# Kernel optimization log

Measured on AMD Instinct MI355X. Metric: run time of the kernel, lower is better.

Reference implementation:

```python
import jax, jax.numpy as jnp
import numpy as np

D, NH, B, N, P = 512, 4, 4096, 30, 30  # embed_dim, num_heads, batch, seq, num_positional_embeddings


def _ln(x, g, b, eps=1e-5):
    mu = jnp.mean(x, axis=-1, keepdims=True)
    var = jnp.mean((x - mu) ** 2, axis=-1, keepdims=True)
    return g * (x - mu) / jnp.sqrt(var + eps) + b


def setup_inputs() -> dict:
    key = jax.random.key(0)
    ks = jax.random.split(key, 8)
    s = 0.02
    x = jax.random.normal(ks[0], (B, N, D), jnp.float32)
    attention_mask = jnp.zeros((B, N), dtype=bool)
    order = jax.random.randint(ks[1], (B, N), 0, P)
    num_docs = jnp.full((B,), float(N), jnp.float32)
    docs_weights = jax.random.uniform(ks[2], (B, N), jnp.float32)
    clusters_centroids = jax.random.normal(ks[3], (B, D), jnp.float32)
    pos_emb = (jax.random.normal(ks[4], (P + 1, D), jnp.float32) * s).at[P].set(0.0)
    fc1_w1 = jax.random.normal(ks[5], (2 * D + 1, D), jnp.float32) * s
    fc1_b1 = jnp.zeros((D,), jnp.float32)
    fc1_w2 = jax.random.normal(ks[6], (D, NH), jnp.float32) * s
    fc1_b2 = jnp.zeros((NH,), jnp.float32)
    fc2_w = jax.random.normal(ks[7], (NH * D, D), jnp.float32) * s
    fc2_b = jnp.zeros((D,), jnp.float32)
    return dict(
        x=x, attention_mask=attention_mask, order=order, num_docs=num_docs,
        docs_weights=docs_weights, clusters_centroids=clusters_centroids,
        pos_emb=pos_emb, fc1_w1=fc1_w1, fc1_b1=fc1_b1, fc1_w2=fc1_w2, fc1_b2=fc1_b2,
        fc2_w=fc2_w, fc2_b=fc2_b,
        ln1_g=jnp.ones((D,), jnp.float32), ln1_b=jnp.zeros((D,), jnp.float32),
        ln2_g=jnp.ones((NH * D,), jnp.float32), ln2_b=jnp.zeros((NH * D,), jnp.float32),
        ln3_g=jnp.ones((D,), jnp.float32), ln3_b=jnp.zeros((D,), jnp.float32),
        ln4_g=jnp.ones((D,), jnp.float32), ln4_b=jnp.zeros((D,), jnp.float32),
    )


def reference(x, attention_mask, order, num_docs, docs_weights, clusters_centroids,
              pos_emb, fc1_w1, fc1_b1, fc1_w2, fc1_b2, fc2_w, fc2_b,
              ln1_g, ln1_b, ln2_g, ln2_b, ln3_g, ln3_b, ln4_g, ln4_b):
    eps = 1e-8
    # norm_1: F.normalize(x, dim=2, eps=1e-8)
    xn = x / jnp.maximum(jnp.linalg.norm(x, axis=2, keepdims=True), eps)
    # input layernorm
    x1 = _ln(xn, ln1_g, ln1_b)
    xp = x1 + pos_emb[order]  # [B,N,D]
    # weighted mean pool of x_positions
    mp = jnp.sum(xp * docs_weights[:, :, None], axis=1, keepdims=True) / num_docs[:, None, None]  # [B,1,D]
    # cosine similarity between mean_pool and each token (torch eps=1e-8)
    num = jnp.sum(mp * xp, axis=2)  # [B,N]
    den = jnp.maximum(jnp.linalg.norm(mp, axis=2) * jnp.linalg.norm(xp, axis=2), eps)
    cos = (num / den)[:, :, None]  # [B,N,1]
    fc1_in = jnp.concatenate([xp, jnp.broadcast_to(mp, xp.shape), cos], axis=2)  # [B,N,2D+1]
    Z = jnp.tanh(fc1_in @ fc1_w1 + fc1_b1) @ fc1_w2 + fc1_b2  # [B,N,H]
    Z = jnp.where(attention_mask[:, :, None], -jnp.inf, Z)
    A = jax.nn.softmax(Z, axis=1)  # [B,N,H]
    b, n, h = A.shape
    d = x1.shape[2]
    # Faithful to the original reshape([B*H, N, 1]) on a [B,N,H]-contiguous tensor
    A_h = A.reshape(b, h, n)
    Hh = jnp.einsum('bhn,bnd->bhd', A_h, x1).reshape(b, h * d)  # [B, H*D]
    # residual: weighted mean pool of x (post ln1), tiled per head
    mpx = jnp.sum(x1 * docs_weights[:, :, None], axis=1) / num_docs[:, None]  # [B,D]
    Hh = _ln(Hh + jnp.tile(mpx, (1, h)), ln2_g, ln2_b)
    pred = _ln(Hh @ fc2_w + fc2_b, ln3_g, ln3_b)  # afterFC layernorm
    pred = _ln(pred + jnp.mean(Hh.reshape(b, h, d), axis=1), ln4_g, ln4_b)
    return pred
```

## Files before the change

### kernel.cpp

```cpp
#include <hip/hip_runtime.h>
#include <hip/hip_bf16.h>

#define B_ 4096
#define N_ 30
#define D_ 512
#define H_ 4
#define M_ (B_*N_)
#define PE_ROWS 31

typedef unsigned short u16;
typedef __attribute__((ext_vector_type(8))) short bf16x8;
typedef __attribute__((ext_vector_type(4))) float f32x4;

__device__ __forceinline__ float bf2f(u16 s) { return __uint_as_float(((unsigned)s) << 16); }
__device__ __forceinline__ u16 f2bf(float f) {
  __hip_bfloat16 h = __float2bfloat16(f);
  return *reinterpret_cast<u16*>(&h);
}

__device__ __forceinline__ float ftanh(float x) {
  float e = __expf(2.f * x);
  return 1.f - 2.f * __builtin_amdgcn_rcpf(e + 1.f);
}

__device__ __forceinline__ void gll16(const void* g, void* l) {
  __builtin_amdgcn_global_load_lds(
      (const __attribute__((address_space(1))) unsigned int*)g,
      (__attribute__((address_space(3))) unsigned int*)l, 16, 0, 0);
}

__device__ __forceinline__ float wsum(float v) {
  #pragma unroll
  for (int m = 32; m >= 1; m >>= 1) v += __shfl_xor(v, m);
  return v;
}
__device__ __forceinline__ float wmax(float v) {
  #pragma unroll
  for (int m = 32; m >= 1; m >>= 1) v = fmaxf(v, __shfl_xor(v, m));
  return v;
}

__global__ __launch_bounds__(512) void k1_prep(
    const float* __restrict__ x, const int* __restrict__ order,
    const float* __restrict__ ndocs, const float* __restrict__ dw,
    const float* __restrict__ pe, const float* __restrict__ g1,
    const float* __restrict__ bln1,
    u16* __restrict__ x1bf, u16* __restrict__ mpbf, float* __restrict__ mpx,
    float* __restrict__ cosb) {
  __shared__ float lds_mp[8*512];
  __shared__ float lds_mpx[8*512];
  __shared__ float xps[32];
  int b = blockIdx.x;
  int tid = threadIdx.x;
  int wid = tid >> 6, lane = tid & 63;
  int d0 = lane * 8;
  float g[8], bl[8];
  *(float4*)&g[0]  = *(const float4*)&g1[d0];
  *(float4*)&g[4]  = *(const float4*)&g1[d0+4];
  *(float4*)&bl[0] = *(const float4*)&bln1[d0];
  *(float4*)&bl[4] = *(const float4*)&bln1[d0+4];
  float xp_reg[4][8];
  float accmp[8] = {0,0,0,0,0,0,0,0}, accmpx[8] = {0,0,0,0,0,0,0,0};
  #pragma unroll
  for (int t = 0; t < 4; ++t) {
    int n = wid + 8*t;
    if (n < N_) {
      int tok = b*N_ + n;
      float v[8];
      *(float4*)&v[0] = *(const float4*)&x[(size_t)tok*D_ + d0];
      *(float4*)&v[4] = *(const float4*)&x[(size_t)tok*D_ + d0 + 4];
      float ss = 0.f, sm = 0.f;
      #pragma unroll
      for (int i = 0; i < 8; ++i) { ss += v[i]*v[i]; sm += v[i]; }
      ss = wsum(ss); sm = wsum(sm);
      float inv = 1.f / fmaxf(sqrtf(ss), 1e-8f);
      float mu = sm * inv * (1.f/D_);
      float m2 = ss*inv*inv*(1.f/D_);
      float rs = 1.f / sqrtf(m2 - mu*mu + 1e-5f);
      int o = order[tok];
      float p8[8];
      *(float4*)&p8[0] = *(const float4*)&pe[(size_t)o*D_ + d0];
      *(float4*)&p8[4] = *(const float4*)&pe[(size_t)o*D_ + d0 + 4];
      float wv = dw[tok];
      float sq = 0.f;
      bf16x8 xb;
      #pragma unroll
      for (int i = 0; i < 8; ++i) {
        float x1v = g[i]*((v[i]*inv - mu)*rs) + bl[i];
        xb[i] = (short)f2bf(x1v);
        float xpv = x1v + p8[i];
        xp_reg[t][i] = xpv;
        accmp[i]  += wv*xpv;
        accmpx[i] += wv*x1v;
        sq += xpv*xpv;
      }
      *(bf16x8*)&x1bf[(size_t)tok*D_ + d0] = xb;
      sq = wsum(sq);
      if (lane == 0) xps[n] = sq;
    }
  }
  #pragma unroll
  for (int i = 0; i < 8; i += 4) {
    *(float4*)&lds_mp[wid*512 + d0 + i]  = *(float4*)&accmp[i];
    *(float4*)&lds_mpx[wid*512 + d0 + i] = *(float4*)&accmpx[i];
  }
  __syncthreads();
  float invnd = 1.f / ndocs[b];
  float mpv[8] = {0,0,0,0,0,0,0,0}, mpxv[8] = {0,0,0,0,0,0,0,0};
  #pragma unroll
  for (int w = 0; w < 8; ++w) {
    #pragma unroll
    for (int i = 0; i < 8; i += 4) {
      float4 a = *(float4*)&lds_mp[w*512 + d0 + i];
      mpv[i+0] += a.x; mpv[i+1] += a.y; mpv[i+2] += a.z; mpv[i+3] += a.w;
      float4 c = *(float4*)&lds_mpx[w*512 + d0 + i];
      mpxv[i+0] += c.x; mpxv[i+1] += c.y; mpxv[i+2] += c.z; mpxv[i+3] += c.w;
    }
  }
  #pragma unroll
  for (int i = 0; i < 8; ++i) { mpv[i] *= invnd; mpxv[i] *= invnd; }
  if (wid == 0) {
    bf16x8 mb;
    #pragma unroll
    for (int i = 0; i < 8; ++i) mb[i] = (short)f2bf(mpv[i]);
    *(bf16x8*)&mpbf[(size_t)b*D_ + d0] = mb;
  }
  if (wid == 1) {
    #pragma unroll
    for (int i = 0; i < 8; i += 4)
      *(float4*)&mpx[(size_t)b*D_ + d0 + i] = *(float4*)&mpxv[i];
  }
  float mn = 0.f;
  #pragma unroll
  for (int i = 0; i < 8; ++i) mn += mpv[i]*mpv[i];
  float mpn = sqrtf(wsum(mn));
  #pragma unroll
  for (int t = 0; t < 4; ++t) {
    int n = wid + 8*t;
    if (n < N_) {
      float dot = 0.f;
      #pragma unroll
      for (int i = 0; i < 8; ++i) dot += mpv[i]*xp_reg[t][i];
      dot = wsum(dot);
      if (lane == 0)
        cosb[b*N_ + n] = dot / fmaxf(mpn * sqrtf(xps[n]), 1e-8f);
    }
  }
}

__global__ __launch_bounds__(512) void k_pew(
    const float* __restrict__ pe, const float* __restrict__ w1,
    float* __restrict__ peW) {
  int p = blockIdx.x, j = threadIdx.x;
  float acc = 0.f;
  for (int dd = 0; dd < D_; ++dd) acc += pe[p*D_ + dd] * w1[(size_t)dd*D_ + j];
  peW[p*D_ + j] = acc;
}

__global__ __launch_bounds__(256) void k_tcvt(
    const float* __restrict__ in, u16* __restrict__ out, int Kdim, int Jdim) {
  __shared__ float tile[64][65];
  int k0 = blockIdx.x * 64, j0 = blockIdx.y * 64;
  int t = threadIdx.x;
  int tr = t >> 4, tc4 = (t & 15) * 4;
  #pragma unroll
  for (int i = 0; i < 4; ++i) {
    int k = k0 + tr + i*16;
    float4 v = *(const float4*)&in[(size_t)k*Jdim + j0 + tc4];
    tile[tr + i*16][tc4+0] = v.x;
    tile[tr + i*16][tc4+1] = v.y;
    tile[tr + i*16][tc4+2] = v.z;
    tile[tr + i*16][tc4+3] = v.w;
  }
  __syncthreads();
  #pragma unroll
  for (int i = 0; i < 4; ++i) {
    int j = tr + i*16;
    uint2 u;
    u.x = (unsigned)f2bf(tile[tc4+0][j]) | ((unsigned)f2bf(tile[tc4+1][j]) << 16);
    u.y = (unsigned)f2bf(tile[tc4+2][j]) | ((unsigned)f2bf(tile[tc4+3][j]) << 16);
    *(uint2*)&out[(size_t)(j0+j)*Kdim + k0 + tc4] = u;
  }
}

__global__ __launch_bounds__(256, 3) void k2_mpw(
    const u16* __restrict__ mpbf, const u16* __restrict__ w1mT,
    const float* __restrict__ b1, float* __restrict__ mpW) {
  __shared__ __align__(16) u16 As[128*64];
  __shared__ __align__(16) u16 Bs[128*64];
  int tid = threadIdx.x;
  int lane = tid & 63, wid = tid >> 6;
  int wg = (blockIdx.x & 7)*16 + (blockIdx.x >> 3);
  int colb = wg & 3, rowb = wg >> 2;
  int row0 = rowb*128, col0 = colb*128;
  int wm = wid >> 1, wn = wid & 1;
  int lr = lane & 15, lk = lane >> 4;
  int srow = lane >> 3;
  int skel = ((lane & 7) ^ srow) << 3;
  f32x4 acc[4][4];
  #pragma unroll
  for (int nf = 0; nf < 4; ++nf) {
    float bv = b1[col0 + wn*64 + nf*16 + lr];
    #pragma unroll
    for (int mf = 0; mf < 4; ++mf)
      acc[mf][nf] = (f32x4){bv, bv, bv, bv};
  }
  for (int k0 = 0; k0 < D_; k0 += 64) {
    __syncthreads();
    #pragma unroll
    for (int i = 0; i < 4; ++i) {
      int rb = wid*32 + i*8;
      gll16(&mpbf[(size_t)(row0 + rb + srow)*D_ + k0 + skel], &As[rb*64]);
      gll16(&w1mT[(size_t)(col0 + rb + srow)*D_ + k0 + skel], &Bs[rb*64]);
    }
    __syncthreads();
    #pragma unroll
    for (int kk = 0; kk < 2; ++kk) {
      int kb = (kk*64 + lk*16) ^ ((lr & 7) << 4);
      bf16x8 a[4];
      #pragma unroll
      for (int mf = 0; mf < 4; ++mf)
        a[mf] = *(const bf16x8*)((const char*)As + (wm*64 + mf*16 + lr)*128 + kb);
      #pragma unroll
      for (int nf = 0; nf < 4; ++nf) {
        bf16x8 bfr = *(const bf16x8*)((const char*)Bs + (wn*64 + nf*16 + lr)*128 + kb);
        #pragma unroll
        for (int mf = 0; mf < 4; ++mf)
          acc[mf][nf] = __builtin_amdgcn_mfma_f32_16x16x32_bf16(a[mf], bfr, acc[mf][nf], 0, 0, 0);
      }
    }
  }
  #pragma unroll
  for (int mf = 0; mf < 4; ++mf)
    #pragma unroll
    for (int nf = 0; nf < 4; ++nf)
      #pragma unroll
      for (int r = 0; r < 4; ++r) {
        int m = row0 + wm*64 + mf*16 + lk*4 + r;
        int j = col0 + wn*64 + nf*16 + lr;
        mpW[(size_t)m*D_ + j] = acc[mf][nf][r];
      }
}

__global__ __launch_bounds__(256, 3) void k4_fc1(
    const u16* __restrict__ x1bf, const u16* __restrict__ w1T,
    const float* __restrict__ w1, const float* __restrict__ w2,
    const int* __restrict__ order, const float* __restrict__ cosb,
    const float* __restrict__ mpW, const float* __restrict__ peW,
    float* __restrict__ Zp) {
  __shared__ __align__(16) u16 As[128*64];
  __shared__ __align__(16) u16 Bs[128*64];
  __shared__ float zred[2*128*4];
  int tid = threadIdx.x;
  int lane = tid & 63, wid = tid >> 6;
  int wg = (blockIdx.x & 7)*480 + (blockIdx.x >> 3);
  int colb = wg & 3, rowb = wg >> 2;
  int col0 = colb * 128;
  int row0 = rowb * 128;
  int wm = wid >> 1, wn = wid & 1;
  int lr = lane & 15, lk = lane >> 4;
  int srow = lane >> 3;
  int skel = ((lane & 7) ^ srow) << 3;
  float wl[4];
  #pragma unroll
  for (int nf = 0; nf < 4; ++nf)
    wl[nf] = w1[(size_t)1024*D_ + col0 + wn*64 + nf*16 + lr];
  f32x4 acc[4][4];
  #pragma unroll
  for (int mf = 0; mf < 4; ++mf) {
    #pragma unroll
    for (int r = 0; r < 4; ++r) {
      int m = row0 + wm*64 + mf*16 + lk*4 + r;
      int bidx = m / N_;
      int o = order[m];
      float cs = cosb[m];
      #pragma unroll
      for (int nf = 0; nf < 4; ++nf) {
        int jl = col0 + wn*64 + nf*16 + lr;
        acc[mf][nf][r] = mpW[(size_t)bidx*D_ + jl] + peW[o*D_ + jl] + cs*wl[nf];
      }
    }
  }
  for (int k0 = 0; k0 < D_; k0 += 64) {
    __syncthreads();
    #pragma unroll
    for (int i = 0; i < 4; ++i) {
      int rb = wid*32 + i*8;
      gll16(&x1bf[(size_t)(row0 + rb + srow)*D_ + k0 + skel], &As[rb*64]);
      gll16(&w1T [(size_t)(col0 + rb + srow)*D_ + k0 + skel], &Bs[rb*64]);
    }
    __syncthreads();
    #pragma unroll
    for (int kk = 0; kk < 2; ++kk) {
      int kb = (kk*64 + lk*16) ^ ((lr & 7) << 4);
      bf16x8 a[4];
      #pragma unroll
      for (int mf = 0; mf < 4; ++mf)
        a[mf] = *(const bf16x8*)((const char*)As + (wm*64 + mf*16 + lr)*128 + kb);
      #pragma unroll
      for (int nf = 0; nf < 4; ++nf) {
        bf16x8 bfr = *(const bf16x8*)((const char*)Bs + (wn*64 + nf*16 + lr)*128 + kb);
        #pragma unroll
        for (int mf = 0; mf < 4; ++mf)
          acc[mf][nf] = __builtin_amdgcn_mfma_f32_16x16x32_bf16(a[mf], bfr, acc[mf][nf], 0, 0, 0);
      }
    }
  }
  float w2r[4][4];
  #pragma unroll
  for (int nf = 0; nf < 4; ++nf)
    *(float4*)w2r[nf] = *(const float4*)&w2[(col0 + wn*64 + nf*16 + lr)*4];
  #pragma unroll
  for (int mf = 0; mf < 4; ++mf) {
    #pragma unroll
    for (int r = 0; r < 4; ++r) {
      int rowt = wm*64 + mf*16 + lk*4 + r;
      float z0=0.f, z1=0.f, z2=0.f, z3=0.f;
      #pragma unroll
      for (int nf = 0; nf < 4; ++nf) {
        float t = ftanh(acc[mf][nf][r]);
        z0 += t * w2r[nf][0]; z1 += t * w2r[nf][1];
        z2 += t * w2r[nf][2]; z3 += t * w2r[nf][3];
      }
      #pragma unroll
      for (int msk = 1; msk <= 8; msk <<= 1) {
        z0 += __shfl_xor(z0, msk); z1 += __shfl_xor(z1, msk);
        z2 += __shfl_xor(z2, msk); z3 += __shfl_xor(z3, msk);
      }
      if (lr == 0)
        *(float4*)&zred[(wn*128 + rowt)*4] = make_float4(z0, z1, z2, z3);
    }
  }
  __syncthreads();
  if (tid < 128) {
    float4 s0 = *(float4*)&zred[tid*4];
    float4 s1 = *(float4*)&zred[(128 + tid)*4];
    *(float4*)&Zp[((size_t)colb*M_ + row0 + tid)*4] =
        make_float4(s0.x+s1.x, s0.y+s1.y, s0.z+s1.z, s0.w+s1.w);
  }
}

__global__ __launch_bounds__(512) void k5_attn(
    const float* __restrict__ Zp, const float* __restrict__ b2,
    const unsigned char* __restrict__ amask, const u16* __restrict__ x1bf,
    const float* __restrict__ mpx, const float* __restrict__ g2,
    const float* __restrict__ bln2, u16* __restrict__ Hh2bf,
    float* __restrict__ hmean) {
  __shared__ float abuf[8][120];
  int tid = threadIdx.x;
  int wid = tid >> 6, lane = tid & 63;
  int b = blockIdx.x*8 + wid;
  bool act = lane < N_;
  int tok = b*N_ + (act ? lane : 0);
  float zz[4] = {-INFINITY, -INFINITY, -INFINITY, -INFINITY};
  if (act) {
    float4 za = *(const float4*)&Zp[(size_t)tok*4];
    float4 zb = *(const float4*)&Zp[((size_t)M_ + tok)*4];
    float4 zc = *(const float4*)&Zp[((size_t)2*M_ + tok)*4];
    float4 zd = *(const float4*)&Zp[((size_t)3*M_ + tok)*4];
    float4 bv = *(const float4*)b2;
    zz[0] = za.x+zb.x+zc.x+zd.x+bv.x; zz[1] = za.y+zb.y+zc.y+zd.y+bv.y;
    zz[2] = za.z+zb.z+zc.z+zd.z+bv.z; zz[3] = za.w+zb.w+zc.w+zd.w+bv.w;
    if (amask[tok]) { zz[0]=zz[1]=zz[2]=zz[3]=-INFINITY; }
  }
  float p[4];
  #pragma unroll
  for (int h = 0; h < 4; ++h) {
    float mx = wmax(zz[h]);
    float e = act ? __expf(zz[h] - mx) : 0.f;
    float s = wsum(e);
    p[h] = e / s;
  }
  if (act) *(float4*)&abuf[wid][lane*4] = make_float4(p[0], p[1], p[2], p[3]);
  __syncthreads();
  float hv[4][8] = {};
  const u16* xr = &x1bf[(size_t)b*N_*D_ + lane*8];
  for (int j = 0; j < N_; ++j) {
    bf16x8 xb = *(const bf16x8*)(xr + (size_t)j*D_);
    float xv[8];
    #pragma unroll
    for (int e = 0; e < 8; ++e) xv[e] = bf2f((u16)xb[e]);
    #pragma unroll
    for (int i = 0; i < 4; ++i) {
      float a = abuf[wid][i*N_ + j];
      #pragma unroll
      for (int e = 0; e < 8; ++e) hv[i][e] += a * xv[e];
    }
  }
  float mpxv[8];
  *(float4*)&mpxv[0] = *(const float4*)&mpx[(size_t)b*D_ + lane*8];
  *(float4*)&mpxv[4] = *(const float4*)&mpx[(size_t)b*D_ + lane*8 + 4];
  float s1 = 0.f, s2 = 0.f;
  #pragma unroll
  for (int i = 0; i < 4; ++i)
    #pragma unroll
    for (int e = 0; e < 8; ++e) {
      hv[i][e] += mpxv[e];
      s1 += hv[i][e];
      s2 += hv[i][e]*hv[i][e];
    }
  s1 = wsum(s1); s2 = wsum(s2);
  float mu = s1 * (1.f/2048.f);
  float var = s2 * (1.f/2048.f) - mu*mu;
  float rs = 1.f / sqrtf(var + 1e-5f);
  float hm[8] = {0,0,0,0,0,0,0,0};
  #pragma unroll
  for (int i = 0; i < 4; ++i) {
    int idx = i*D_ + lane*8;
    float gg[8], bb[8];
    *(float4*)&gg[0] = *(const float4*)&g2[idx];
    *(float4*)&gg[4] = *(const float4*)&g2[idx+4];
    *(float4*)&bb[0] = *(const float4*)&bln2[idx];
    *(float4*)&bb[4] = *(const float4*)&bln2[idx+4];
    bf16x8 ob;
    #pragma unroll
    for (int e = 0; e < 8; ++e) {
      float v = gg[e]*((hv[i][e]-mu)*rs) + bb[e];
      hm[e] += v;
      ob[e] = (short)f2bf(v);
    }
    *(bf16x8*)&Hh2bf[(size_t)b*2048 + idx] = ob;
  }
  #pragma unroll
  for (int e = 0; e < 8; ++e) hm[e] *= 0.25f;
  *(float4*)&hmean[(size_t)b*D_ + lane*8]     = *(float4*)&hm[0];
  *(float4*)&hmean[(size_t)b*D_ + lane*8 + 4] = *(float4*)&hm[4];
}

__global__ __launch_bounds__(256, 3) void k6_fc2(
    const u16* __restrict__ Hh2bf, const u16* __restrict__ fwT,
    float* __restrict__ pred_p) {
  __shared__ __align__(16) u16 As[128*64];
  __shared__ __align__(16) u16 Bs[128*64];
  int tid = threadIdx.x;
  int lane = tid & 63, wid = tid >> 6;
  int wg = (blockIdx.x & 7)*64 + (blockIdx.x >> 3);
  int kz = wg >> 7;
  int rem = wg & 127;
  int rowb = rem >> 2, colb = rem & 3;
  int row0 = rowb*128, col0 = colb*128;
  int kbase = kz*512;
  int wm = wid >> 1, wn = wid & 1;
  int lr = lane & 15, lk = lane >> 4;
  int srow = lane >> 3;
  int skel = ((lane & 7) ^ srow) << 3;
  f32x4 acc[4][4] = {};
  for (int k0 = kbase; k0 < kbase + 512; k0 += 64) {
    __syncthreads();
    #pragma unroll
    for (int i = 0; i < 4; ++i) {
      int rb = wid*32 + i*8;
      gll16(&Hh2bf[(size_t)(row0 + rb + srow)*2048 + k0 + skel], &As[rb*64]);
      gll16(&fwT  [(size_t)(col0 + rb + srow)*2048 + k0 + skel], &Bs[rb*64]);
    }
    __syncthreads();
    #pragma unroll
    for (int kk = 0; kk < 2; ++kk) {
      int kb = (kk*64 + lk*16) ^ ((lr & 7) << 4);
      bf16x8 a[4];
      #pragma unroll
      for (int mf = 0; mf < 4; ++mf)
        a[mf] = *(const bf16x8*)((const char*)As + (wm*64 + mf*16 + lr)*128 + kb);
      #pragma unroll
      for (int nf = 0; nf < 4; ++nf) {
        bf16x8 bfr = *(const bf16x8*)((const char*)Bs + (wn*64 + nf*16 + lr)*128 + kb);
        #pragma unroll
        for (int mf = 0; mf < 4; ++mf)
          acc[mf][nf] = __builtin_amdgcn_mfma_f32_16x16x32_bf16(a[mf], bfr, acc[mf][nf], 0, 0, 0);
      }
    }
  }
  float* dst = pred_p + (size_t)kz * B_ * D_;
  #pragma unroll
  for (int mf = 0; mf < 4; ++mf)
    #pragma unroll
    for (int nf = 0; nf < 4; ++nf)
      #pragma unroll
      for (int r = 0; r < 4; ++r) {
        int m = row0 + wm*64 + mf*16 + lk*4 + r;
        int j = col0 + wn*64 + nf*16 + lr;
        dst[(size_t)m*D_ + j] = acc[mf][nf][r];
      }
}

__global__ __launch_bounds__(512) void k7_final(
    const float* __restrict__ pred_p, const float* __restrict__ hmean,
    const float* __restrict__ fb,
    const float* __restrict__ g3, const float* __restrict__ b3,
    const float* __restrict__ g4, const float* __restrict__ b4,
    float* __restrict__ out) {
  int tid = threadIdx.x;
  int wid = tid >> 6, lane = tid & 63;
  int b = blockIdx.x*8 + wid;
  int d0 = lane*8;
  size_t i = (size_t)b*D_ + d0;
  size_t BD = (size_t)B_*D_;
  float p[8];
  #pragma unroll
  for (int e = 0; e < 8; e += 4) {
    float4 a0 = *(const float4*)&pred_p[i+e];
    float4 a1 = *(const float4*)&pred_p[BD+i+e];
    float4 a2 = *(const float4*)&pred_p[2*BD+i+e];
    float4 a3 = *(const float4*)&pred_p[3*BD+i+e];
    float4 fv = *(const float4*)&fb[d0+e];
    p[e+0] = a0.x+a1.x+a2.x+a3.x+fv.x;
    p[e+1] = a0.y+a1.y+a2.y+a3.y+fv.y;
    p[e+2] = a0.z+a1.z+a2.z+a3.z+fv.z;
    p[e+3] = a0.w+a1.w+a2.w+a3.w+fv.w;
  }
  float s1 = 0.f, s2 = 0.f;
  #pragma unroll
  for (int e = 0; e < 8; ++e) { s1 += p[e]; s2 += p[e]*p[e]; }
  s1 = wsum(s1); s2 = wsum(s2);
  float mu = s1*(1.f/D_);
  float var = s2*(1.f/D_) - mu*mu;
  float rs = 1.f / sqrtf(var + 1e-5f);
  float g3v[8], b3v[8], hmv[8], q[8];
  *(float4*)&g3v[0] = *(const float4*)&g3[d0];
  *(float4*)&g3v[4] = *(const float4*)&g3[d0+4];
  *(float4*)&b3v[0] = *(const float4*)&b3[d0];
  *(float4*)&b3v[4] = *(const float4*)&b3[d0+4];
  *(float4*)&hmv[0] = *(const float4*)&hmean[i];
  *(float4*)&hmv[4] = *(const float4*)&hmean[i+4];
  float t1 = 0.f, t2 = 0.f;
  #pragma unroll
  for (int e = 0; e < 8; ++e) {
    q[e] = g3v[e]*((p[e]-mu)*rs) + b3v[e] + hmv[e];
    t1 += q[e]; t2 += q[e]*q[e];
  }
  t1 = wsum(t1); t2 = wsum(t2);
  mu = t1*(1.f/D_);
  var = t2*(1.f/D_) - mu*mu;
  rs = 1.f / sqrtf(var + 1e-5f);
  float g4v[8], b4v[8], o[8];
  *(float4*)&g4v[0] = *(const float4*)&g4[d0];
  *(float4*)&g4v[4] = *(const float4*)&g4[d0+4];
  *(float4*)&b4v[0] = *(const float4*)&b4[d0];
  *(float4*)&b4v[4] = *(const float4*)&b4[d0+4];
  #pragma unroll
  for (int e = 0; e < 8; ++e) o[e] = g4v[e]*((q[e]-mu)*rs) + b4v[e];
  *(float4*)&out[i]   = *(float4*)&o[0];
  *(float4*)&out[i+4] = *(float4*)&o[4];
}

extern "C" void kernel_launch(void* const* d_in, const int* in_sizes, int n_in,
                              void* d_out, int out_size, void* d_ws, size_t ws_size,
                              hipStream_t stream) {
  const float* x      = (const float*)d_in[0];
  const unsigned char* amask = (const unsigned char*)d_in[1];
  const int*   order  = (const int*)d_in[2];
  const float* ndocs  = (const float*)d_in[3];
  const float* dw     = (const float*)d_in[4];
  const float* pe     = (const float*)d_in[6];
  const float* w1     = (const float*)d_in[7];
  const float* b1     = (const float*)d_in[8];
  const float* w2     = (const float*)d_in[9];
  const float* b2     = (const float*)d_in[10];
  const float* fw     = (const float*)d_in[11];
  const float* fb     = (const float*)d_in[12];
  const float* g1     = (const float*)d_in[13];
  const float* bln1   = (const float*)d_in[14];
  const float* g2     = (const float*)d_in[15];
  const float* bln2   = (const float*)d_in[16];
  const float* g3     = (const float*)d_in[17];
  const float* b3     = (const float*)d_in[18];
  const float* g4     = (const float*)d_in[19];
  const float* b4     = (const float*)d_in[20];
  float* out = (float*)d_out;

  char* ws = (char*)d_ws;
  size_t off = 0;
  u16*   x1bf   = (u16*)(ws + off);   off += (size_t)M_*D_*2;
  u16*   mpbf   = (u16*)(ws + off);   off += (size_t)B_*D_*2;
  float* mpx    = (float*)(ws + off); off += (size_t)B_*D_*4;
  float* mpW    = (float*)(ws + off); off += (size_t)B_*D_*4;
  float* hmean  = (float*)(ws + off); off += (size_t)B_*D_*4;
  float* peW    = (float*)(ws + off); off += (size_t)PE_ROWS*D_*4;
  float* cosb   = (float*)(ws + off); off += (size_t)M_*4;
  float* Zp     = (float*)(ws + off); off += (size_t)4*M_*4*4;
  float* pred_p = (float*)(ws + off); off += (size_t)4*B_*D_*4;
  u16*   Hh2bf  = (u16*)(ws + off);   off += (size_t)B_*2048*2;
  u16*   w1T    = (u16*)(ws + off);   off += (size_t)D_*D_*2;
  u16*   w1mT   = (u16*)(ws + off);   off += (size_t)D_*D_*2;
  u16*   fwT    = (u16*)(ws + off);   off += (size_t)D_*2048*2;
  (void)ws_size; (void)in_sizes; (void)n_in; (void)out_size;

  k_tcvt<<<dim3(8, 8), 256, 0, stream>>>(w1, w1T, 512, 512);
  k_tcvt<<<dim3(8, 8), 256, 0, stream>>>(w1 + 512*512, w1mT, 512, 512);
  k_tcvt<<<dim3(32, 8), 256, 0, stream>>>(fw, fwT, 2048, 512);
  k_pew<<<PE_ROWS, 512, 0, stream>>>(pe, w1, peW);
  k1_prep<<<B_, 512, 0, stream>>>(x, order, ndocs, dw, pe, g1, bln1,
                                  x1bf, mpbf, mpx, cosb);
  k2_mpw<<<128, 256, 0, stream>>>(mpbf, w1mT, b1, mpW);
  k4_fc1<<<3840, 256, 0, stream>>>(x1bf, w1T, w1, w2, order, cosb,
                                   mpW, peW, Zp);
  k5_attn<<<B_/8, 512, 0, stream>>>(Zp, b2, amask, x1bf, mpx, g2, bln2,
                                    Hh2bf, hmean);
  k6_fc2<<<512, 256, 0, stream>>>(Hh2bf, fwT, pred_p);
  k7_final<<<B_/8, 512, 0, stream>>>(pred_p, hmean, fb, g3, b3, g4, b4, out);
}
```

Measured before the change: 328.6 us.

## Merge weight transpose, PE projection and prep into one kernel; raise GEMM occupancy

Folds the three weight transpose-convert launches and the positional-embedding projection into the prep kernel as extra blocks, so five launches become one and the small kernels run alongside the per-batch prep work. The PE projection now stages its pe row in LDS. The fc1 and fc2 GEMMs get a launch-bounds minimum of 4 blocks per CU instead of 3, which may force register spilling.

```diff
diff --git a/kernel.cpp b/kernel.cpp
--- a/kernel.cpp
+++ b/kernel.cpp
@@ -40,18 +40,55 @@
   return v;
 }
 
-__global__ __launch_bounds__(512) void k1_prep(
+__global__ __launch_bounds__(512) void k1_mega(
     const float* __restrict__ x, const int* __restrict__ order,
     const float* __restrict__ ndocs, const float* __restrict__ dw,
     const float* __restrict__ pe, const float* __restrict__ g1,
     const float* __restrict__ bln1,
+    const float* __restrict__ w1, const float* __restrict__ fw,
     u16* __restrict__ x1bf, u16* __restrict__ mpbf, float* __restrict__ mpx,
-    float* __restrict__ cosb) {
-  __shared__ float lds_mp[8*512];
-  __shared__ float lds_mpx[8*512];
-  __shared__ float xps[32];
-  int b = blockIdx.x;
+    float* __restrict__ cosb,
+    u16* __restrict__ w1T, u16* __restrict__ w1mT, u16* __restrict__ fwT,
+    float* __restrict__ peW) {
+  __shared__ __align__(16) char smem[32896];
+  int bid = blockIdx.x;
   int tid = threadIdx.x;
+  if (bid >= B_) {
+    int r = bid - B_;
+    if (r < 384) {
+      const float* in; u16* outp; int Kdim, Jdim, bx, by;
+      if (r < 64)       { in = w1;            outp = w1T;  Kdim = 512;  Jdim = 512;  bx = r >> 3;        by = r & 7; }
+      else if (r < 128) { in = w1 + 512*512;  outp = w1mT; Kdim = 512;  Jdim = 512;  bx = (r-64) >> 3;   by = (r-64) & 7; }
+      else              { in = fw;            outp = fwT;  Kdim = 2048; Jdim = 512;  bx = (r-128) >> 3;  by = (r-128) & 7; }
+      int k0 = bx*64, j0 = by*64;
+      float* tile = (float*)smem;
+      int rowk = tid >> 3, c8 = (tid & 7) * 8;
+      float4 v0 = *(const float4*)&in[(size_t)(k0+rowk)*Jdim + j0 + c8];
+      float4 v1 = *(const float4*)&in[(size_t)(k0+rowk)*Jdim + j0 + c8 + 4];
+      float* tr = tile + rowk*65;
+      tr[c8+0]=v0.x; tr[c8+1]=v0.y; tr[c8+2]=v0.z; tr[c8+3]=v0.w;
+      tr[c8+4]=v1.x; tr[c8+5]=v1.y; tr[c8+6]=v1.z; tr[c8+7]=v1.w;
+      __syncthreads();
+      int j = tid >> 3, k8 = (tid & 7) * 8;
+      u16 tmp[8];
+      #pragma unroll
+      for (int i = 0; i < 8; ++i) tmp[i] = f2bf(tile[(k8+i)*65 + j]);
+      *(uint4*)&outp[(size_t)(j0+j)*Kdim + k0 + k8] = *(uint4*)tmp;
+    } else {
+      int p = r - 384;
+      float* pes = (float*)smem;
+      pes[tid] = pe[(size_t)p*D_ + tid];
+      __syncthreads();
+      float acc = 0.f;
+      for (int dd = 0; dd < D_; ++dd) acc += pes[dd] * w1[(size_t)dd*D_ + tid];
+      peW[p*D_ + tid] = acc;
+    }
+    return;
+  }
+  float* lds_mp  = (float*)smem;
+  float* lds_mpx = lds_mp + 8*512;
+  float* xps     = lds_mpx + 8*512;
+  int b = bid;
   int wid = tid >> 6, lane = tid & 63;
   int d0 = lane * 8;
   float g[8], bl[8];
@@ -145,41 +182,6 @@
       if (lane == 0)
         cosb[b*N_ + n] = dot / fmaxf(mpn * sqrtf(xps[n]), 1e-8f);
     }
-  }
-}
-
-__global__ __launch_bounds__(512) void k_pew(
-    const float* __restrict__ pe, const float* __restrict__ w1,
-    float* __restrict__ peW) {
-  int p = blockIdx.x, j = threadIdx.x;
-  float acc = 0.f;
-  for (int dd = 0; dd < D_; ++dd) acc += pe[p*D_ + dd] * w1[(size_t)dd*D_ + j];
-  peW[p*D_ + j] = acc;
-}
-
-__global__ __launch_bounds__(256) void k_tcvt(
-    const float* __restrict__ in, u16* __restrict__ out, int Kdim, int Jdim) {
-  __shared__ float tile[64][65];
-  int k0 = blockIdx.x * 64, j0 = blockIdx.y * 64;
-  int t = threadIdx.x;
-  int tr = t >> 4, tc4 = (t & 15) * 4;
-  #pragma unroll
-  for (int i = 0; i < 4; ++i) {
-    int k = k0 + tr + i*16;
-    float4 v = *(const float4*)&in[(size_t)k*Jdim + j0 + tc4];
-    tile[tr + i*16][tc4+0] = v.x;
-    tile[tr + i*16][tc4+1] = v.y;
-    tile[tr + i*16][tc4+2] = v.z;
-    tile[tr + i*16][tc4+3] = v.w;
-  }
-  __syncthreads();
-  #pragma unroll
-  for (int i = 0; i < 4; ++i) {
-    int j = tr + i*16;
-    uint2 u;
-    u.x = (unsigned)f2bf(tile[tc4+0][j]) | ((unsigned)f2bf(tile[tc4+1][j]) << 16);
-    u.y = (unsigned)f2bf(tile[tc4+2][j]) | ((unsigned)f2bf(tile[tc4+3][j]) << 16);
-    *(uint2*)&out[(size_t)(j0+j)*Kdim + k0 + tc4] = u;
   }
 }
 
@@ -242,7 +244,7 @@
       }
 }
 
-__global__ __launch_bounds__(256, 3) void k4_fc1(
+__global__ __launch_bounds__(256, 4) void k4_fc1(
     const u16* __restrict__ x1bf, const u16* __restrict__ w1T,
     const float* __restrict__ w1, const float* __restrict__ w2,
     const int* __restrict__ order, const float* __restrict__ cosb,
@@ -427,7 +429,7 @@
   *(float4*)&hmean[(size_t)b*D_ + lane*8 + 4] = *(float4*)&hm[4];
 }
 
-__global__ __launch_bounds__(256, 3) void k6_fc2(
+__global__ __launch_bounds__(256, 4) void k6_fc2(
     const u16* __restrict__ Hh2bf, const u16* __restrict__ fwT,
     float* __restrict__ pred_p) {
   __shared__ __align__(16) u16 As[128*64];
@@ -585,12 +587,9 @@
   u16*   fwT    = (u16*)(ws + off);   off += (size_t)D_*2048*2;
   (void)ws_size; (void)in_sizes; (void)n_in; (void)out_size;
 
-  k_tcvt<<<dim3(8, 8), 256, 0, stream>>>(w1, w1T, 512, 512);
-  k_tcvt<<<dim3(8, 8), 256, 0, stream>>>(w1 + 512*512, w1mT, 512, 512);
-  k_tcvt<<<dim3(32, 8), 256, 0, stream>>>(fw, fwT, 2048, 512);
-  k_pew<<<PE_ROWS, 512, 0, stream>>>(pe, w1, peW);
-  k1_prep<<<B_, 512, 0, stream>>>(x, order, ndocs, dw, pe, g1, bln1,
-                                  x1bf, mpbf, mpx, cosb);
+  k1_mega<<<B_ + 384 + PE_ROWS, 512, 0, stream>>>(
+      x, order, ndocs, dw, pe, g1, bln1, w1, fw,
+      x1bf, mpbf, mpx, cosb, w1T, w1mT, fwT, peW);
   k2_mpw<<<128, 256, 0, stream>>>(mpbf, w1mT, b1, mpW);
   k4_fc1<<<3840, 256, 0, stream>>>(x1bf, w1T, w1, w2, order, cosb,
                                    mpW, peW, Zp);
```

Result: faster. 289.9 us (-11.8%).
